# Optimization experiments

Measured on AMD Instinct MI355X. Metric: run time of the kernel, lower is better.

Reference implementation:

```python
import jax, jax.numpy as jnp
import numpy as np

N_POINTS = 200000
B, H, W, K = 16, 299, 299, 8


def setup_inputs() -> dict:
    key = jax.random.key(0)
    k1, k2, k3, k4 = jax.random.split(key, 4)
    spatial_rgb = jax.random.normal(k1, (N_POINTS, 4), dtype=jnp.float32)
    weights = jax.random.uniform(k2, (B, H, W, K), dtype=jnp.float32)
    idx = jax.random.randint(k3, (B, H, W, K), 0, N_POINTS).astype(jnp.float32)
    weight_and_index_list = jnp.stack([weights, idx], axis=1)  # (B,2,H,W,K)
    ori_img = jax.random.uniform(k4, (B, H, W, 4), dtype=jnp.float32) * 255.0
    return {"spatial_rgb": spatial_rgb,
            "weight_and_index_list": weight_and_index_list,
            "ori_img": ori_img}


def reference(spatial_rgb, weight_and_index_list, ori_img):
    # s: flat (N,4) RGBA table
    s = spatial_rgb.reshape(-1, 4)
    w = weight_and_index_list[:, 0]                      # (B,H,W,K) weights
    idx = weight_and_index_list[:, 1].astype(jnp.int32)  # (B,H,W,K) flat indices

    # gather (B,H,W,K,4), weighted sum over K -> (B,H,W,4)
    gathered = s[idx]
    x = jnp.sum(gathered * w[..., None], axis=-2)

    alpha = x[..., 3:4] / 255.0          # (B,H,W,1)
    ori_alpha = ori_img[..., 3:4]

    # epsilon is None -> unclipped branch
    x_rgb = ori_img[..., :3] + x[..., :3] * alpha
    x_rgb = jnp.where(ori_alpha > 0, x_rgb, jnp.zeros_like(x_rgb))
    x_rgba = jnp.clip(jnp.concatenate([x_rgb, ori_alpha], axis=-1), 0.0, 255.0)

    # NHWC -> NCHW (transpose(2,3).transpose(1,2))
    cla_x = jnp.transpose(x_rgba, (0, 3, 1, 2))
    cla_ori = jnp.transpose(ori_img, (0, 3, 1, 2))

    def alpha_to_white(img_nchw):
        a = img_nchw[:, 3:4]
        return jnp.where(a > 0, img_nchw[:, :3], jnp.full_like(img_nchw[:, :3], 255.0))

    # model_name == 'my_model': no resize; classifier stubbed as identity
    cla = alpha_to_white(cla_x)
    ori_cla = alpha_to_white(cla_ori)
    return (x, x_rgba, cla, ori_img, ori_cla)
```

## Files before the change

### kernel.cpp

```cpp
#include <hip/hip_runtime.h>

#define BB 16
#define HH 299
#define WW 299
#define KK 8
#define HWPIX (HH * WW)
#define NPIX (BB * HWPIX)
#define PPT 2
#define TPB 256
#define SPAN (TPB * PPT)

typedef float f4 __attribute__((ext_vector_type(4)));

__global__ __launch_bounds__(TPB) void gauss_net_kernel(
    const f4* __restrict__ spatial,
    const f4* __restrict__ wi4,
    const f4* __restrict__ ori,
    float* __restrict__ out)
{
    const int tbase = blockIdx.x * SPAN + threadIdx.x;

    f4*    out_x    = (f4*)out;
    f4*    out_rgba = out_x + NPIX;
    float* out_cla  = (float*)(out_rgba + NPIX);
    f4*    out_ori  = (f4*)(out_cla + (size_t)BB * 3 * HWPIX);
    float* out_ocla = (float*)(out_ori + NPIX);

    int  p[PPT], bidx[PPT], rem[PPT];
    bool act[PPT];
    f4   w0[PPT], w1[PPT], i0[PPT], i1[PPT], o[PPT];

#pragma unroll
    for (int u = 0; u < PPT; ++u) {
        p[u]   = tbase + u * TPB;
        act[u] = (p[u] < NPIX);
        int pc = act[u] ? p[u] : 0;
        bidx[u] = pc / HWPIX;
        rem[u]  = pc - bidx[u] * HWPIX;
        size_t wb = ((size_t)(2 * bidx[u]) * HWPIX + rem[u]) * 2;
        size_t ib = wb + (size_t)HWPIX * 2;
        w0[u] = __builtin_nontemporal_load(wi4 + wb);
        w1[u] = __builtin_nontemporal_load(wi4 + wb + 1);
        i0[u] = __builtin_nontemporal_load(wi4 + ib);
        i1[u] = __builtin_nontemporal_load(wi4 + ib + 1);
        o[u]  = __builtin_nontemporal_load(ori + pc);
    }

    f4 g[PPT][KK];
#pragma unroll
    for (int u = 0; u < PPT; ++u) {
        int id[KK] = { (int)i0[u].x, (int)i0[u].y, (int)i0[u].z, (int)i0[u].w,
                       (int)i1[u].x, (int)i1[u].y, (int)i1[u].z, (int)i1[u].w };
#pragma unroll
        for (int k = 0; k < KK; ++k) g[u][k] = spatial[id[k]];
    }

#pragma unroll
    for (int u = 0; u < PPT; ++u) {
        if (!act[u]) continue;
        float wt[KK] = { w0[u].x, w0[u].y, w0[u].z, w0[u].w,
                         w1[u].x, w1[u].y, w1[u].z, w1[u].w };
        f4 acc = (f4){0.f, 0.f, 0.f, 0.f};
#pragma unroll
        for (int k = 0; k < KK; ++k) acc += g[u][k] * wt[k];

        f4 ov = o[u];
        float alpha = acc.w * (1.0f / 255.0f);
        float r  = fmaf(acc.x, alpha, ov.x);
        float gr = fmaf(acc.y, alpha, ov.y);
        float bl = fmaf(acc.z, alpha, ov.z);
        bool oa_pos = (ov.w > 0.0f);
        if (!oa_pos) { r = 0.f; gr = 0.f; bl = 0.f; }

        float cr = fminf(fmaxf(r,  0.f), 255.f);
        float cg = fminf(fmaxf(gr, 0.f), 255.f);
        float cb = fminf(fmaxf(bl, 0.f), 255.f);
        float ca = fminf(fmaxf(ov.w, 0.f), 255.f);

        __builtin_nontemporal_store(acc, out_x + p[u]);
        __builtin_nontemporal_store((f4){cr, cg, cb, ca}, out_rgba + p[u]);
        __builtin_nontemporal_store(ov, out_ori + p[u]);

        size_t cbase = (size_t)bidx[u] * 3 * HWPIX + rem[u];
        bool ca_pos = (ca > 0.0f);
        __builtin_nontemporal_store(ca_pos ? cr : 255.0f, out_cla + cbase);
        __builtin_nontemporal_store(ca_pos ? cg : 255.0f, out_cla + cbase + HWPIX);
        __builtin_nontemporal_store(ca_pos ? cb : 255.0f, out_cla + cbase + 2 * HWPIX);

        __builtin_nontemporal_store(oa_pos ? ov.x : 255.0f, out_ocla + cbase);
        __builtin_nontemporal_store(oa_pos ? ov.y : 255.0f, out_ocla + cbase + HWPIX);
        __builtin_nontemporal_store(oa_pos ? ov.z : 255.0f, out_ocla + cbase + 2 * HWPIX);
    }
}

extern "C" void kernel_launch(void* const* d_in, const int* in_sizes, int n_in,
                              void* d_out, int out_size, void* d_ws, size_t ws_size,
                              hipStream_t stream) {
    const f4* spatial = (const f4*)d_in[0];
    const f4* wi4     = (const f4*)d_in[1];
    const f4* ori     = (const f4*)d_in[2];
    float* out = (float*)d_out;

    int blocks = (NPIX + SPAN - 1) / SPAN;
    gauss_net_kernel<<<blocks, TPB, 0, stream>>>(spatial, wi4, ori, out);
}
```

Before: 233.9 us.

## Use persistent grid-stride loop with software-prefetched streaming loads

Replaces the one-shot launch (two pixels per thread) with a fixed grid of 768 blocks that loop over pixels in grid-stride fashion. Each iteration prefetches the next pixel's weight, index and image vectors while the current pixel's gathers and stores are in flight, so streaming loads overlap the random gathers. The aim is to hide memory latency with explicit pipelining instead of relying on many resident waves, at the cost of fewer resident waves and less memory-level parallelism per thread.

New measurement: 235.2 us. About the same (+0.6%).

```diff
diff --git a/kernel.cpp b/kernel.cpp
--- a/kernel.cpp
+++ b/kernel.cpp
@@ -1,4 +1,5 @@
 #include <hip/hip_runtime.h>
+#include <stdint.h>
 
 #define BB 16
 #define HH 299
@@ -6,19 +7,38 @@
 #define KK 8
 #define HWPIX (HH * WW)
 #define NPIX (BB * HWPIX)
-#define PPT 2
 #define TPB 256
-#define SPAN (TPB * PPT)
+#define GRID 768
+#define GSPAN (GRID * TPB)
+#define ITERS ((NPIX + GSPAN - 1) / GSPAN)
 
 typedef float f4 __attribute__((ext_vector_type(4)));
 
-__global__ __launch_bounds__(TPB) void gauss_net_kernel(
+struct Streams { f4 w0, w1, i0, i1, o; };
+
+static __device__ __forceinline__ Streams load_streams(
+    const f4* __restrict__ wi4, const f4* __restrict__ ori, int p, bool act) {
+    int pc = act ? p : 0;
+    int b   = pc / HWPIX;
+    int rem = pc - b * HWPIX;
+    size_t wb = ((size_t)(2 * b) * HWPIX + rem) * 2;
+    size_t ib = wb + (size_t)HWPIX * 2;
+    Streams s;
+    s.w0 = __builtin_nontemporal_load(wi4 + wb);
+    s.w1 = __builtin_nontemporal_load(wi4 + wb + 1);
+    s.i0 = __builtin_nontemporal_load(wi4 + ib);
+    s.i1 = __builtin_nontemporal_load(wi4 + ib + 1);
+    s.o  = __builtin_nontemporal_load(ori + pc);
+    return s;
+}
+
+__global__ __launch_bounds__(TPB, 3) void gauss_net_kernel(
     const f4* __restrict__ spatial,
     const f4* __restrict__ wi4,
     const f4* __restrict__ ori,
     float* __restrict__ out)
 {
-    const int tbase = blockIdx.x * SPAN + threadIdx.x;
+    const int tid = blockIdx.x * TPB + threadIdx.x;
 
     f4*    out_x    = (f4*)out;
     f4*    out_rgba = out_x + NPIX;
@@ -26,70 +46,60 @@
     f4*    out_ori  = (f4*)(out_cla + (size_t)BB * 3 * HWPIX);
     float* out_ocla = (float*)(out_ori + NPIX);
 
-    int  p[PPT], bidx[PPT], rem[PPT];
-    bool act[PPT];
-    f4   w0[PPT], w1[PPT], i0[PPT], i1[PPT], o[PPT];
+    Streams cur = load_streams(wi4, ori, tid, tid < NPIX);
 
+#pragma unroll 1
+    for (int it = 0; it < ITERS; ++it) {
+        const int  p   = it * GSPAN + tid;
+        const bool act = (p < NPIX);
+
+        int id[KK] = { (int)cur.i0.x, (int)cur.i0.y, (int)cur.i0.z, (int)cur.i0.w,
+                       (int)cur.i1.x, (int)cur.i1.y, (int)cur.i1.z, (int)cur.i1.w };
+        f4 g[KK];
 #pragma unroll
-    for (int u = 0; u < PPT; ++u) {
-        p[u]   = tbase + u * TPB;
-        act[u] = (p[u] < NPIX);
-        int pc = act[u] ? p[u] : 0;
-        bidx[u] = pc / HWPIX;
-        rem[u]  = pc - bidx[u] * HWPIX;
-        size_t wb = ((size_t)(2 * bidx[u]) * HWPIX + rem[u]) * 2;
-        size_t ib = wb + (size_t)HWPIX * 2;
-        w0[u] = __builtin_nontemporal_load(wi4 + wb);
-        w1[u] = __builtin_nontemporal_load(wi4 + wb + 1);
-        i0[u] = __builtin_nontemporal_load(wi4 + ib);
-        i1[u] = __builtin_nontemporal_load(wi4 + ib + 1);
-        o[u]  = __builtin_nontemporal_load(ori + pc);
-    }
+        for (int k = 0; k < KK; ++k) g[k] = spatial[id[k]];
 
-    f4 g[PPT][KK];
-#pragma unroll
-    for (int u = 0; u < PPT; ++u) {
-        int id[KK] = { (int)i0[u].x, (int)i0[u].y, (int)i0[u].z, (int)i0[u].w,
-                       (int)i1[u].x, (int)i1[u].y, (int)i1[u].z, (int)i1[u].w };
-#pragma unroll
-        for (int k = 0; k < KK; ++k) g[u][k] = spatial[id[k]];
-    }
+        const int pn = p + GSPAN;
+        Streams nxt = load_streams(wi4, ori, pn, pn < NPIX);
 
-#pragma unroll
-    for (int u = 0; u < PPT; ++u) {
-        if (!act[u]) continue;
-        float wt[KK] = { w0[u].x, w0[u].y, w0[u].z, w0[u].w,
-                         w1[u].x, w1[u].y, w1[u].z, w1[u].w };
+        float wt[KK] = { cur.w0.x, cur.w0.y, cur.w0.z, cur.w0.w,
+                         cur.w1.x, cur.w1.y, cur.w1.z, cur.w1.w };
         f4 acc = (f4){0.f, 0.f, 0.f, 0.f};
 #pragma unroll
-        for (int k = 0; k < KK; ++k) acc += g[u][k] * wt[k];
+        for (int k = 0; k < KK; ++k) acc += g[k] * wt[k];
 
-        f4 ov = o[u];
-        float alpha = acc.w * (1.0f / 255.0f);
-        float r  = fmaf(acc.x, alpha, ov.x);
-        float gr = fmaf(acc.y, alpha, ov.y);
-        float bl = fmaf(acc.z, alpha, ov.z);
-        bool oa_pos = (ov.w > 0.0f);
-        if (!oa_pos) { r = 0.f; gr = 0.f; bl = 0.f; }
+        if (act) {
+            const int b   = p / HWPIX;
+            const int rem = p - b * HWPIX;
+            f4 ov = cur.o;
+            float alpha = acc.w * (1.0f / 255.0f);
+            float r  = fmaf(acc.x, alpha, ov.x);
+            float gr = fmaf(acc.y, alpha, ov.y);
+            float bl = fmaf(acc.z, alpha, ov.z);
+            bool oa_pos = (ov.w > 0.0f);
+            if (!oa_pos) { r = 0.f; gr = 0.f; bl = 0.f; }
 
-        float cr = fminf(fmaxf(r,  0.f), 255.f);
-        float cg = fminf(fmaxf(gr, 0.f), 255.f);
-        float cb = fminf(fmaxf(bl, 0.f), 255.f);
-        float ca = fminf(fmaxf(ov.w, 0.f), 255.f);
+            float cr = fminf(fmaxf(r,  0.f), 255.f);
+            float cg = fminf(fmaxf(gr, 0.f), 255.f);
+            float cb = fminf(fmaxf(bl, 0.f), 255.f);
+            float ca = fminf(fmaxf(ov.w, 0.f), 255.f);
 
-        __builtin_nontemporal_store(acc, out_x + p[u]);
-        __builtin_nontemporal_store((f4){cr, cg, cb, ca}, out_rgba + p[u]);
-        __builtin_nontemporal_store(ov, out_ori + p[u]);
+            __builtin_nontemporal_store(acc, out_x + p);
+            __builtin_nontemporal_store((f4){cr, cg, cb, ca}, out_rgba + p);
+            __builtin_nontemporal_store(ov, out_ori + p);
 
-        size_t cbase = (size_t)bidx[u] * 3 * HWPIX + rem[u];
-        bool ca_pos = (ca > 0.0f);
-        __builtin_nontemporal_store(ca_pos ? cr : 255.0f, out_cla + cbase);
-        __builtin_nontemporal_store(ca_pos ? cg : 255.0f, out_cla + cbase + HWPIX);
-        __builtin_nontemporal_store(ca_pos ? cb : 255.0f, out_cla + cbase + 2 * HWPIX);
+            size_t cbase = (size_t)b * 3 * HWPIX + rem;
+            bool ca_pos = (ca > 0.0f);
+            __builtin_nontemporal_store(ca_pos ? cr : 255.0f, out_cla + cbase);
+            __builtin_nontemporal_store(ca_pos ? cg : 255.0f, out_cla + cbase + HWPIX);
+            __builtin_nontemporal_store(ca_pos ? cb : 255.0f, out_cla + cbase + 2 * HWPIX);
 
-        __builtin_nontemporal_store(oa_pos ? ov.x : 255.0f, out_ocla + cbase);
-        __builtin_nontemporal_store(oa_pos ? ov.y : 255.0f, out_ocla + cbase + HWPIX);
-        __builtin_nontemporal_store(oa_pos ? ov.z : 255.0f, out_ocla + cbase + 2 * HWPIX);
+            __builtin_nontemporal_store(oa_pos ? ov.x : 255.0f, out_ocla + cbase);
+            __builtin_nontemporal_store(oa_pos ? ov.y : 255.0f, out_ocla + cbase + HWPIX);
+            __builtin_nontemporal_store(oa_pos ? ov.z : 255.0f, out_ocla + cbase + 2 * HWPIX);
+        }
+
+        cur = nxt;
     }
 }
 
@@ -101,6 +111,5 @@
     const f4* ori     = (const f4*)d_in[2];
     float* out = (float*)d_out;
 
-    int blocks = (NPIX + SPAN - 1) / SPAN;
-    gauss_net_kernel<<<blocks, TPB, 0, stream>>>(spatial, wi4, ori, out);
+    gauss_net_kernel<<<GRID, TPB, 0, stream>>>(spatial, wi4, ori, out);
 }
```
